# Kernel optimization log

Measured on AMD Instinct MI355X. Metric: run time of the kernel, lower is better.

## Reference

```python
import jax, jax.numpy as jnp
import numpy as np

B, CIN, H, W = 4, 256, 128, 128   # x1/x2 each [B, CIN, H, W]
C2 = 2 * CIN                       # 512, channels after concat
CQK = CIN // 8                     # 32, query/key channels


def setup_inputs() -> dict:
    key = jax.random.key(0)
    ks = jax.random.split(key, 12)
    s = 0.02
    return {
        "x1": jax.random.normal(ks[0], (B, CIN, H, W), jnp.float32),
        "x2": jax.random.normal(ks[1], (B, CIN, H, W), jnp.float32),
        # 1x1 convs as [out,in] matrices + bias
        "Wq": jax.random.normal(ks[2], (CQK, C2), jnp.float32) * s,
        "bq": jnp.zeros((CQK,), jnp.float32),
        "Wk": jax.random.normal(ks[3], (CQK, C2), jnp.float32) * s,
        "bk": jnp.zeros((CQK,), jnp.float32),
        "Wv": jax.random.normal(ks[4], (C2, C2), jnp.float32) * s,
        "bv": jnp.zeros((C2,), jnp.float32),
        "Wm": jax.random.normal(ks[5], (C2, C2), jnp.float32) * s,
        "bm": jnp.zeros((C2,), jnp.float32),
        "gamma": jnp.zeros((1,), jnp.float32),
    }


def _conv1x1(w, b, x):
    # x: [b,c,h,w] -> [b,o,h,w]
    return jnp.einsum('oc,bchw->bohw', w, x) + b[None, :, None, None]


def reference(x1, x2, Wq, bq, Wk, bk, Wv, bv, Wm, bm, gamma):
    b, _, h, w = x1.shape
    x = jnp.concatenate([x1, x2], axis=1)          # [b, 2C, h, w]
    q = _conv1x1(Wq, bq, x)                        # [b, cqk, h, w]
    k = _conv1x1(Wk, bk, x)                        # [b, cqk, h, w]
    v = _conv1x1(Wv, bv, x)                        # [b, 2C, h, w]

    # column (H-axis) energy: [b, h_q, w, h_k], diagonal h_q==h_k masked to -inf
    energy_H = jnp.einsum('bciw,bcjw->biwj', q, k)
    diag = jnp.eye(h, dtype=bool)[None, :, None, :]
    energy_H = jnp.where(diag, -jnp.inf, energy_H)
    # row (W-axis) energy: [b, h, w_q, w_k]
    energy_W = jnp.einsum('bchi,bchj->bhij', q, k)

    concate = jax.nn.softmax(jnp.concatenate([energy_H, energy_W], axis=3), axis=3)
    att_H = concate[..., :h]                       # [b, h_q, w, h_k]
    att_W = concate[..., h:]                       # [b, h, w_q, w_k]

    out_H = jnp.einsum('bcjw,biwj->bciw', v, att_H)  # [b, 2C, h, w]
    out_W = jnp.einsum('bchj,bhij->bchi', v, att_W)  # [b, 2C, h, w]

    out = gamma[0] * (out_H + out_W) + x
    out = _conv1x1(Wm, bm, out)                    # [b, 2C, h, w]
    out = out.reshape(b, 2, C2 // 2, h, w).transpose(1, 0, 2, 3, 4)
    return out
```

## Files before the change

### kernel.cpp

```cpp
#include <hip/hip_runtime.h>
#include <cstdint>

#define HW 16384
#define HH 128
#define WW 128
#define C2 512
#define CQK 32
#define NB_TOT 4

typedef unsigned short u16;
typedef unsigned int u32;

using bf16x8 = __attribute__((ext_vector_type(8))) short;
using f32x4  = __attribute__((ext_vector_type(4))) float;

__device__ __forceinline__ float us2f(u16 u) { return __uint_as_float(((u32)u) << 16); }
__device__ __forceinline__ u16 f2us(float f) {
    u32 u = __float_as_uint(f);
    u = u + 0x7fffu + ((u >> 16) & 1u);
    return (u16)(u >> 16);
}
__device__ __forceinline__ u32 pack2(float a, float b) {
    return (u32)f2us(a) | ((u32)f2us(b) << 16);
}
__device__ __forceinline__ void unpack8(uint4 p, float* f) {
    u32 a[4] = {p.x, p.y, p.z, p.w};
#pragma unroll
    for (int q = 0; q < 4; ++q) {
        f[q * 2 + 0] = __uint_as_float(a[q] << 16);
        f[q * 2 + 1] = __uint_as_float(a[q] & 0xffff0000u);
    }
}
union U8 { uint4 v; u16 s[8]; };

__device__ __forceinline__ void gl_lds16(const void* g, const void* lds) {
    __builtin_amdgcn_global_load_lds(
        (const __attribute__((address_space(1))) unsigned int*)g,
        (__attribute__((address_space(3))) unsigned int*)lds, 16, 0, 0);
}

__global__ __launch_bounds__(256) void convert_weights(
    const float* __restrict__ Wq, const float* __restrict__ Wk,
    const float* __restrict__ Wv, const float* __restrict__ Wm,
    u16* __restrict__ Wall)
{
    int id = blockIdx.x * 256 + threadIdx.x;
    if (id >= 1088 * 128) return;
    int row = id >> 7, q4 = id & 127;
    const float* src;
    if (row < 32) src = Wq + (size_t)row * 512;
    else if (row < 64) src = Wk + (size_t)(row - 32) * 512;
    else if (row < 576) src = Wv + (size_t)(row - 64) * 512;
    else src = Wm + (size_t)(row - 576) * 512;
    float4 v = *reinterpret_cast<const float4*>(src + q4 * 4);
    alignas(8) u16 h[4] = {f2us(v.x), f2us(v.y), f2us(v.z), f2us(v.w)};
    *reinterpret_cast<uint2*>(Wall + (size_t)row * 512 + q4 * 4) =
        *reinterpret_cast<uint2*>(h);
}

__global__ __launch_bounds__(512) void conv_final(
    const u16* __restrict__ Wmb, const float* __restrict__ bm,
    const float* __restrict__ x1, const float* __restrict__ x2,
    const u16* __restrict__ y, float* __restrict__ out,
    int b0, const float* __restrict__ gamma)
{
    __shared__ u16 As[512 * 64];
    __shared__ u32 Ps[64 * 36];
    const int t = threadIdx.x, lane = t & 63, wid = t >> 6;
    const int bz = blockIdx.z, bg = b0 + bz;
    const int p0 = blockIdx.x * 64;
    const int l15 = lane & 15, l16 = lane >> 4;
    const bool useY = (gamma[0] != 0.f);
    const int pcol = t & 15, cpair = t >> 4;
    const u16* yb = y + (size_t)bz * C2 * HW;

    f32x4 acc[4][4];
#pragma unroll
    for (int i = 0; i < 4; ++i)
#pragma unroll
        for (int j = 0; j < 4; ++j) acc[i][j] = (f32x4)0.f;

    for (int k0 = 0; k0 < 512; k0 += 64) {
        __syncthreads();
#pragma unroll
        for (int it = 0; it < 8; ++it) {
            int sflat = it * 512 + t;
            int m = sflat >> 3, slot = sflat & 7;
            int ck = slot ^ (m & 7);
            gl_lds16(Wmb + (size_t)m * 512 + k0 + ck * 8, As + sflat * 8);
        }
        {
            const int ce = k0 + cpair * 2, co = ce + 1;
            if (useY) {
                const u16* s0 = yb + (size_t)ce * HW + p0;
                const u16* s1 = yb + (size_t)co * HW + p0;
#pragma unroll
                for (int i = 0; i < 4; ++i) {
                    int p = pcol + i * 16;
                    Ps[p * 36 + cpair] = (u32)s0[p] | ((u32)s1[p] << 16);
                }
            } else {
                const float* s0 = (ce < 256) ? x1 + ((size_t)bg * 256 + ce) * HW + p0
                                             : x2 + ((size_t)bg * 256 + ce - 256) * HW + p0;
                const float* s1 = (co < 256) ? x1 + ((size_t)bg * 256 + co) * HW + p0
                                             : x2 + ((size_t)bg * 256 + co - 256) * HW + p0;
#pragma unroll
                for (int i = 0; i < 4; ++i) {
                    int p = pcol + i * 16;
                    Ps[p * 36 + cpair] = pack2(s0[p], s1[p]);
                }
            }
        }
        __syncthreads();
#pragma unroll
        for (int kk = 0; kk < 2; ++kk) {
            bf16x8 af[4], bfq[4];
#pragma unroll
            for (int mi = 0; mi < 4; ++mi) {
                int row = wid * 64 + mi * 16 + l15;
                int slot = (kk * 4 + l16) ^ (row & 7);
                af[mi] = *(const bf16x8*)&As[row * 64 + slot * 8];
            }
#pragma unroll
            for (int ni = 0; ni < 4; ++ni) {
                int p = ni * 16 + l15;
                bfq[ni] = *(const bf16x8*)((const u16*)&Ps[p * 36 + kk * 16 + l16 * 4]);
            }
#pragma unroll
            for (int mi = 0; mi < 4; ++mi)
#pragma unroll
                for (int ni = 0; ni < 4; ++ni)
                    acc[mi][ni] = __builtin_amdgcn_mfma_f32_16x16x32_bf16(
                        af[mi], bfq[ni], acc[mi][ni], 0, 0, 0);
        }
    }
#pragma unroll
    for (int mi = 0; mi < 4; ++mi)
#pragma unroll
        for (int ni = 0; ni < 4; ++ni) {
            const int p = p0 + ni * 16 + l15;
#pragma unroll
            for (int r = 0; r < 4; ++r) {
                const int m = wid * 64 + mi * 16 + l16 * 4 + r;
                const float val = acc[mi][ni][r] + bm[m];
                out[(((size_t)(m >> 8) * NB_TOT + bg) * 256 + (m & 255)) * HW + p] = val;
            }
        }
}

__global__ __launch_bounds__(256) void transpose_x(
    const float* __restrict__ x1, const float* __restrict__ x2,
    u16* __restrict__ xT, int b0, const float* __restrict__ gamma)
{
    if (gamma[0] == 0.f) return;
    __shared__ u16 tile[32][33];
    const int bz = blockIdx.z, bg = b0 + bz;
    const int p0 = blockIdx.x * 32;
    const int tx = threadIdx.x, ty = threadIdx.y;
    for (int cy = 0; cy < 16; ++cy) {
        const int c0 = cy * 32;
#pragma unroll
        for (int u = 0; u < 4; ++u) {
            int c = c0 + ty + u * 8;
            const float* xs = (c < 256) ? x1 + ((size_t)bg * 256 + c) * HW
                                        : x2 + ((size_t)bg * 256 + (c - 256)) * HW;
            tile[ty + u * 8][tx] = f2us(xs[p0 + tx]);
        }
        __syncthreads();
#pragma unroll
        for (int u = 0; u < 4; ++u) {
            int p = p0 + ty + u * 8;
            xT[((size_t)bz * HW + p) * 512 + c0 + tx] = tile[tx][ty + u * 8];
        }
        __syncthreads();
    }
}

template <int BM, int MODE>
__global__ __launch_bounds__(256) void conv_mfma(
    const u16* __restrict__ Wb, const float* __restrict__ bias0,
    const float* __restrict__ bias1, const u16* __restrict__ xT,
    float* __restrict__ oQ, float* __restrict__ oK,
    u16* __restrict__ oV, int b0, const float* __restrict__ gamma)
{
    if (gamma[0] == 0.f) return;
    constexpr int FM = BM / 32;
    __shared__ u16 As[BM * 64];
    __shared__ u16 Ps[128 * 64];
    const int t = threadIdx.x, lane = t & 63, wid = t >> 6;
    const int wr = wid >> 1, wc = wid & 1;
    const int bz = blockIdx.z;
    const int p0 = blockIdx.x * 128, m0 = blockIdx.y * BM;
    const u16* xTb = xT + (size_t)bz * HW * 512;
    const int l15 = lane & 15, l16 = lane >> 4;

    f32x4 acc[FM][4];
#pragma unroll
    for (int i = 0; i < FM; ++i)
#pragma unroll
        for (int j = 0; j < 4; ++j) acc[i][j] = (f32x4)0.f;

    for (int c0 = 0; c0 < 512; c0 += 64) {
#pragma unroll
        for (int it = 0; it < BM / 32; ++it) {
            int flat = it * 256 + t;
            int row = flat >> 3, part = flat & 7;
            gl_lds16(Wb + (size_t)(m0 + row) * 512 + c0 + part * 8,
                     As + (it * 256 + wid * 64) * 8);
        }
#pragma unroll
        for (int it = 0; it < 4; ++it) {
            int flat = it * 256 + t;
            int row = flat >> 3, part = flat & 7;
            gl_lds16(xTb + (size_t)(p0 + row) * 512 + c0 + part * 8,
                     Ps + (it * 256 + wid * 64) * 8);
        }
        __syncthreads();
#pragma unroll
        for (int kk = 0; kk < 2; ++kk) {
            bf16x8 af[FM], bfr[4];
#pragma unroll
            for (int mi = 0; mi < FM; ++mi)
                af[mi] = *(const bf16x8*)&As[(wr * (BM / 2) + mi * 16 + l15) * 64 + kk * 32 + l16 * 8];
#pragma unroll
            for (int ni = 0; ni < 4; ++ni)
                bfr[ni] = *(const bf16x8*)&Ps[(wc * 64 + ni * 16 + l15) * 64 + kk * 32 + l16 * 8];
#pragma unroll
            for (int mi = 0; mi < FM; ++mi)
#pragma unroll
                for (int ni = 0; ni < 4; ++ni)
                    acc[mi][ni] = __builtin_amdgcn_mfma_f32_16x16x32_bf16(
                        af[mi], bfr[ni], acc[mi][ni], 0, 0, 0);
        }
        __syncthreads();
    }
#pragma unroll
    for (int mi = 0; mi < FM; ++mi)
#pragma unroll
        for (int ni = 0; ni < 4; ++ni) {
            const int p = p0 + wc * 64 + ni * 16 + l15;
#pragma unroll
            for (int r = 0; r < 4; ++r) {
                const int m = m0 + wr * (BM / 2) + mi * 16 + l16 * 4 + r;
                float val = acc[mi][ni][r];
                if (MODE == 0) {
                    if (m < 32) {
                        val += bias0[m];
                        oQ[((size_t)bz * 32 + m) * HW + p] = val;
                    } else {
                        val += bias1[m - 32];
                        oK[((size_t)bz * 32 + (m - 32)) * HW + p] = val;
                    }
                } else {
                    val += bias0[m];
                    oV[((size_t)bz * 512 + m) * HW + p] = f2us(val);
                }
            }
        }
}

__global__ __launch_bounds__(256) void transpose_bf16(
    const u16* __restrict__ in, u16* __restrict__ out,
    const float* __restrict__ gamma)
{
    if (gamma[0] == 0.f) return;
    __shared__ u16 tile[32][33];
    const int x0 = blockIdx.x * 32, y0 = blockIdx.y * 32;
    const int tx = threadIdx.x, ty = threadIdx.y;
    for (int pp = 0; pp < 16; ++pp) {
        const int plane = blockIdx.z * 16 + pp;
        const u16* ip = in + (size_t)plane * HW;
        u16* op = out + (size_t)plane * HW;
#pragma unroll
        for (int u = 0; u < 4; ++u)
            tile[ty + u * 8][tx] = ip[(size_t)(y0 + ty + u * 8) * WW + x0 + tx];
        __syncthreads();
#pragma unroll
        for (int u = 0; u < 4; ++u)
            op[(size_t)(x0 + ty + u * 8) * HH + y0 + tx] = tile[tx][ty + u * 8];
        __syncthreads();
    }
}

__global__ __launch_bounds__(256) void energy_h_kernel(
    const float* __restrict__ q, const float* __restrict__ k,
    u16* __restrict__ EHt, const float* __restrict__ gamma)
{
    if (gamma[0] == 0.f) return;
    const int w = blockIdx.x, bz = blockIdx.y, t = threadIdx.x;
    __shared__ float qc[32][128];
    __shared__ float kc[32][128];
    __shared__ u16 es[128][128];
    for (int it = 0; it < 16; ++it) {
        int idx = it * 256 + t;
        int c = idx >> 7, j = idx & 127;
        qc[c][j] = q[((size_t)bz * CQK + c) * HW + j * WW + w];
        kc[c][j] = k[((size_t)bz * CQK + c) * HW + j * WW + w];
    }
    __syncthreads();
    const int i = t & 127, half = t >> 7, j0 = half * 64;
    float qi[32];
#pragma unroll
    for (int c = 0; c < 32; ++c) qi[c] = qc[c][i];
    for (int j = j0; j < j0 + 64; ++j) {
        float acc = 0.f;
#pragma unroll
        for (int c = 0; c < 32; ++c) acc += qi[c] * kc[c][j];
        es[i][j] = f2us(i == j ? -1e30f : acc);
    }
    __syncthreads();
    u16* dst = EHt + ((size_t)bz * WW + w) * HW;
    for (int it = 0; it < 8; ++it) {
        int ii = it * 16 + (t >> 4), jj = (t & 15) * 8;
        *reinterpret_cast<uint4*>(&dst[(size_t)ii * HH + jj]) =
            *reinterpret_cast<const uint4*>(&es[ii][jj]);
    }
}

__global__ __launch_bounds__(256) void ew_softmax_ow_kernel(
    const float* __restrict__ q, const float* __restrict__ k,
    const u16* __restrict__ v, u16* __restrict__ EHt,
    u16* __restrict__ oW, const float* __restrict__ gamma)
{
    if (gamma[0] == 0.f) return;
    const int r = blockIdx.x, bz = blockIdx.y, t = threadIdx.x;
    __shared__ float qr[32][128];
    __shared__ float kr[32][128];
    __shared__ u16 ewT[128][136];
    __shared__ u16 vstageT[128][40];
    __shared__ float invA[128];
    __shared__ float red[2][2][128];

    for (int it = 0; it < 16; ++it) {
        int idx = it * 256 + t, c = idx >> 7, j = idx & 127;
        qr[c][j] = q[((size_t)bz * CQK + c) * HW + r * WW + j];
        kr[c][j] = k[((size_t)bz * CQK + c) * HW + r * WW + j];
    }
    __syncthreads();
    const int i = t & 127, half = t >> 7, j0 = half * 64;
    {
        float qi[32];
#pragma unroll
        for (int c = 0; c < 32; ++c) qi[c] = qr[c][i];
        for (int j = j0; j < j0 + 64; ++j) {
            float acc = 0.f;
#pragma unroll
            for (int c = 0; c < 32; ++c) acc += qi[c] * kr[c][j];
            ewT[j][i] = f2us(acc);
        }
    }
    __syncthreads();
    float eh[64];
    u16* ehrow = EHt + (((size_t)bz * WW + i) * HH + r) * HH + j0;
#pragma unroll
    for (int uq = 0; uq < 8; ++uq) {
        uint4 pk = *reinterpret_cast<const uint4*>(ehrow + uq * 8);
        unpack8(pk, eh + uq * 8);
    }
    float m = -3e38f;
#pragma unroll
    for (int u = 0; u < 64; ++u) m = fmaxf(m, eh[u]);
    for (int j = j0; j < j0 + 64; ++j) m = fmaxf(m, us2f(ewT[j][i]));
    red[0][half][i] = m;
    __syncthreads();
    m = fmaxf(red[0][0][i], red[0][1][i]);
    float s = 0.f;
#pragma unroll
    for (int u = 0; u < 64; ++u) { float e = __expf(eh[u] - m); eh[u] = e; s += e; }
    for (int j = j0; j < j0 + 64; ++j) {
        float e = __expf(us2f(ewT[j][i]) - m);
        ewT[j][i] = f2us(e);
        s += e;
    }
    red[1][half][i] = s;
    __syncthreads();
    const float inv = 1.f / (red[1][0][i] + red[1][1][i]);
    if (half == 0) invA[i] = inv;
#pragma unroll
    for (int uq = 0; uq < 8; ++uq) {
        alignas(16) u16 tmp[8];
#pragma unroll
        for (int e = 0; e < 8; ++e) tmp[e] = f2us(eh[uq * 8 + e] * inv);
        *reinterpret_cast<uint4*>(ehrow + uq * 8) = *reinterpret_cast<uint4*>(tmp);
    }
    const int cg = half;
    for (int c0 = 0; c0 < C2; c0 += 32) {
        __syncthreads();
        for (int it = 0; it < 16; ++it) {
            int idx = it * 256 + t, cc = idx >> 7, j = idx & 127;
            vstageT[j][cc] = v[((size_t)bz * C2 + c0 + cc) * HW + r * WW + j];
        }
        __syncthreads();
        float acc[16] = {};
        for (int j = 0; j < 128; ++j) {
            float a = us2f(ewT[j][i]);
            uint4 pq0 = *reinterpret_cast<const uint4*>(&vstageT[j][cg * 16]);
            uint4 pq1 = *reinterpret_cast<const uint4*>(&vstageT[j][cg * 16 + 8]);
            float vv[16];
            unpack8(pq0, vv);
            unpack8(pq1, vv + 8);
#pragma unroll
            for (int u = 0; u < 16; ++u) acc[u] += a * vv[u];
        }
        const float scale = invA[i];
#pragma unroll
        for (int u = 0; u < 16; ++u) {
            int c = c0 + cg * 16 + u;
            oW[((size_t)bz * C2 + c) * HW + r * WW + i] = f2us(acc[u] * scale);
        }
    }
}

__global__ __launch_bounds__(256) void apply_h_kernel(
    const u16* __restrict__ EHt, const u16* __restrict__ vT,
    u16* __restrict__ oHT, const float* __restrict__ gamma)
{
    if (gamma[0] == 0.f) return;
    const int w = blockIdx.x, bz = blockIdx.y, t = threadIdx.x;
    __shared__ u16 aT[128][136];
    __shared__ u16 vstageT[128][40];
    const u16* src = EHt + ((size_t)bz * WW + w) * HW;
    for (int it = 0; it < 8; ++it) {
        int oct = it * 256 + t;
        int ii = oct >> 4, jj = (oct & 15) * 8;
        U8 uu;
        uu.v = *reinterpret_cast<const uint4*>(src + (size_t)ii * HH + jj);
#pragma unroll
        for (int e = 0; e < 8; ++e) aT[jj + e][ii] = uu.s[e];
    }
    const int i = t & 127, cg = t >> 7;
    for (int c0 = 0; c0 < C2; c0 += 32) {
        __syncthreads();
        for (int it = 0; it < 16; ++it) {
            int idx = it * 256 + t, cc = idx >> 7, j = idx & 127;
            vstageT[j][cc] = vT[((size_t)bz * C2 + c0 + cc) * HW + w * HH + j];
        }
        __syncthreads();
        float acc[16] = {};
        for (int j = 0; j < 128; ++j) {
            float a = us2f(aT[j][i]);
            uint4 pq0 = *reinterpret_cast<const uint4*>(&vstageT[j][cg * 16]);
            uint4 pq1 = *reinterpret_cast<const uint4*>(&vstageT[j][cg * 16 + 8]);
            float vv[16];
            unpack8(pq0, vv);
            unpack8(pq1, vv + 8);
#pragma unroll
            for (int u = 0; u < 16; ++u) acc[u] += a * vv[u];
        }
#pragma unroll
        for (int u = 0; u < 16; ++u) {
            int c = c0 + cg * 16 + u;
            oHT[((size_t)bz * C2 + c) * HW + w * HH + i] = f2us(acc[u]);
        }
    }
}

__global__ __launch_bounds__(256) void merge_transpose_kernel(
    const u16* __restrict__ oHT, const u16* __restrict__ oW,
    const float* __restrict__ x1, const float* __restrict__ x2,
    const float* __restrict__ gamma, u16* __restrict__ y, int b0)
{
    const float g = gamma[0];
    if (g == 0.f) return;
    __shared__ float tile[32][33];
    const int w0 = blockIdx.x * 32, i0 = blockIdx.y * 32;
    const int tx = threadIdx.x, ty = threadIdx.y;
    for (int pp = 0; pp < 16; ++pp) {
        const int idx = blockIdx.z * 16 + pp;
        const int c = idx & 511, bz = idx >> 9;
        const int bg = b0 + bz;
        const u16* ih = oHT + ((size_t)bz * C2 + c) * HW;
#pragma unroll
        for (int u = 0; u < 4; ++u)
            tile[ty + u * 8][tx] = us2f(ih[(size_t)(w0 + ty + u * 8) * HH + i0 + tx]);
        __syncthreads();
        const float* xs = (c < 256) ? (x1 + ((size_t)bg * 256 + c) * HW)
                                    : (x2 + ((size_t)bg * 256 + (c - 256)) * HW);
        const u16* ow = oW + ((size_t)bz * C2 + c) * HW;
        u16* yy = y + ((size_t)bz * C2 + c) * HW;
#pragma unroll
        for (int u = 0; u < 4; ++u) {
            int i = i0 + ty + u * 8, w = w0 + tx;
            float oh = tile[tx][ty + u * 8];
            float val = g * (oh + us2f(ow[(size_t)i * WW + w])) + xs[(size_t)i * WW + w];
            yy[(size_t)i * WW + w] = f2us(val);
        }
        __syncthreads();
    }
}

extern "C" void kernel_launch(void* const* d_in, const int* in_sizes, int n_in,
                              void* d_out, int out_size, void* d_ws, size_t ws_size,
                              hipStream_t stream)
{
    const float* x1 = (const float*)d_in[0];
    const float* x2 = (const float*)d_in[1];
    const float* Wq = (const float*)d_in[2];
    const float* bq = (const float*)d_in[3];
    const float* Wk = (const float*)d_in[4];
    const float* bk = (const float*)d_in[5];
    const float* Wv = (const float*)d_in[6];
    const float* bv = (const float*)d_in[7];
    const float* Wm = (const float*)d_in[8];
    const float* bm = (const float*)d_in[9];
    const float* gamma = (const float*)d_in[10];
    float* out = (float*)d_out;

    auto algn = [](size_t v) { return (v + 255) & ~(size_t)255; };
    const size_t wallSz = algn((size_t)1088 * 512 * 2);
    auto need = [&](int nb) -> size_t {
        size_t s = wallSz;
        s += algn((size_t)nb * HW * 512 * 2);
        s += 2 * algn((size_t)nb * 32 * HW * 4);
        s += algn((size_t)nb * C2 * HW * 2);
        s += algn((size_t)nb * C2 * HW * 2);
        s += algn((size_t)nb * WW * HW * 2);
        s += algn((size_t)nb * C2 * HW * 2);
        s += algn((size_t)nb * C2 * HW * 2);
        return s;
    };
    const int nb = (ws_size >= need(4)) ? 4 : (ws_size >= need(2)) ? 2 : 1;

    char* base = (char*)d_ws;
    u16* Wall = (u16*)base; base += wallSz;
    const u16* Wqk = Wall;
    const u16* Wvb = Wall + (size_t)64 * 512;
    const u16* Wmb = Wall + (size_t)576 * 512;

    convert_weights<<<(1088 * 128 + 255) / 256, 256, 0, stream>>>(Wq, Wk, Wv, Wm, Wall);

    for (int b0 = 0; b0 < NB_TOT; b0 += nb) {
        char* p = base;
        u16* xT   = (u16*)p;   p += algn((size_t)nb * HW * 512 * 2);
        float* q  = (float*)p; p += algn((size_t)nb * 32 * HW * 4);
        float* kk = (float*)p; p += algn((size_t)nb * 32 * HW * 4);
        u16* v    = (u16*)p;   p += algn((size_t)nb * C2 * HW * 2);
        u16* vT   = (u16*)p;   p += algn((size_t)nb * C2 * HW * 2);
        u16* EHt  = (u16*)p;   p += algn((size_t)nb * WW * HW * 2);
        u16* oW   = (u16*)p;   p += algn((size_t)nb * C2 * HW * 2);
        u16* oHT  = (u16*)p;   p += algn((size_t)nb * C2 * HW * 2);
        u16* y    = vT;

        transpose_x<<<dim3(HW / 32, 1, nb), dim3(32, 8), 0, stream>>>(
            x1, x2, xT, b0, gamma);
        conv_mfma<64, 0><<<dim3(HW / 128, 1, nb), 256, 0, stream>>>(
            Wqk, bq, bk, xT, q, kk, nullptr, b0, gamma);
        conv_mfma<128, 1><<<dim3(HW / 128, 4, nb), 256, 0, stream>>>(
            Wvb, bv, nullptr, xT, nullptr, nullptr, v, b0, gamma);
        transpose_bf16<<<dim3(4, 4, nb * 32), dim3(32, 8), 0, stream>>>(v, vT, gamma);
        energy_h_kernel<<<dim3(WW, nb), 256, 0, stream>>>(q, kk, EHt, gamma);
        ew_softmax_ow_kernel<<<dim3(HH, nb), 256, 0, stream>>>(q, kk, v, EHt, oW, gamma);
        apply_h_kernel<<<dim3(WW, nb), 256, 0, stream>>>(EHt, vT, oHT, gamma);
        merge_transpose_kernel<<<dim3(4, 4, nb * 32), dim3(32, 8), 0, stream>>>(
            oHT, oW, x1, x2, gamma, y, b0);
        conv_final<<<dim3(HW / 64, 1, nb), 512, 0, stream>>>(
            Wmb, bm, x1, x2, y, out, b0, gamma);
    }
}
```

Measured before the change: 104.0 us.

## Double-buffer weight tiles and widen pixel tile in final conv

The final 1x1 conv kernel now processes 128 pixels per block instead of 64, doubling the accumulator tile per wave so each loaded weight fragment is reused across twice as many MFMAs. It also double-buffers the weight tile in LDS and prefetches the next activation slice into registers while the current slice is being multiplied, hiding global load latency behind compute. The cost is much larger LDS use (two 64KB weight buffers), more accumulator and staging registers, and half as many blocks, all of which may reduce occupancy.

```diff
diff --git a/kernel.cpp b/kernel.cpp
--- a/kernel.cpp
+++ b/kernel.cpp
@@ -64,86 +64,110 @@
     const u16* __restrict__ y, float* __restrict__ out,
     int b0, const float* __restrict__ gamma)
 {
-    __shared__ u16 As[512 * 64];
-    __shared__ u32 Ps[64 * 36];
+    __shared__ u16 As[2][512 * 64];
+    __shared__ u32 Ps[128 * 36];
     const int t = threadIdx.x, lane = t & 63, wid = t >> 6;
     const int bz = blockIdx.z, bg = b0 + bz;
-    const int p0 = blockIdx.x * 64;
+    const int p0 = blockIdx.x * 128;
     const int l15 = lane & 15, l16 = lane >> 4;
     const bool useY = (gamma[0] != 0.f);
     const int pcol = t & 15, cpair = t >> 4;
     const u16* yb = y + (size_t)bz * C2 * HW;
 
-    f32x4 acc[4][4];
+    f32x4 acc[4][8];
 #pragma unroll
     for (int i = 0; i < 4; ++i)
 #pragma unroll
-        for (int j = 0; j < 4; ++j) acc[i][j] = (f32x4)0.f;
-
-    for (int k0 = 0; k0 < 512; k0 += 64) {
-        __syncthreads();
+        for (int j = 0; j < 8; ++j) acc[i][j] = (f32x4)0.f;
+
+    u32 xr[16];
+
+    auto stageW = [&](int k0, int b) {
 #pragma unroll
         for (int it = 0; it < 8; ++it) {
             int sflat = it * 512 + t;
             int m = sflat >> 3, slot = sflat & 7;
             int ck = slot ^ (m & 7);
-            gl_lds16(Wmb + (size_t)m * 512 + k0 + ck * 8, As + sflat * 8);
-        }
-        {
-            const int ce = k0 + cpair * 2, co = ce + 1;
-            if (useY) {
-                const u16* s0 = yb + (size_t)ce * HW + p0;
-                const u16* s1 = yb + (size_t)co * HW + p0;
-#pragma unroll
-                for (int i = 0; i < 4; ++i) {
-                    int p = pcol + i * 16;
-                    Ps[p * 36 + cpair] = (u32)s0[p] | ((u32)s1[p] << 16);
-                }
-            } else {
-                const float* s0 = (ce < 256) ? x1 + ((size_t)bg * 256 + ce) * HW + p0
-                                             : x2 + ((size_t)bg * 256 + ce - 256) * HW + p0;
-                const float* s1 = (co < 256) ? x1 + ((size_t)bg * 256 + co) * HW + p0
-                                             : x2 + ((size_t)bg * 256 + co - 256) * HW + p0;
-#pragma unroll
-                for (int i = 0; i < 4; ++i) {
-                    int p = pcol + i * 16;
-                    Ps[p * 36 + cpair] = pack2(s0[p], s1[p]);
-                }
+            gl_lds16(Wmb + (size_t)m * 512 + k0 + ck * 8, &As[b][sflat * 8]);
+        }
+    };
+    auto loadX = [&](int k0) {
+        const int ce = k0 + cpair * 2;
+        if (useY) {
+            const u16* s0 = yb + (size_t)ce * HW + p0;
+            const u16* s1 = s0 + HW;
+#pragma unroll
+            for (int i = 0; i < 8; ++i) {
+                int p = pcol + i * 16;
+                xr[i] = s0[p]; xr[8 + i] = s1[p];
             }
-        }
-        __syncthreads();
+        } else {
+            const float* s0 = (ce < 256) ? x1 + ((size_t)bg * 256 + ce) * HW + p0
+                                         : x2 + ((size_t)bg * 256 + ce - 256) * HW + p0;
+            const float* s1 = s0 + HW;
+#pragma unroll
+            for (int i = 0; i < 8; ++i) {
+                int p = pcol + i * 16;
+                xr[i] = __float_as_uint(s0[p]);
+                xr[8 + i] = __float_as_uint(s1[p]);
+            }
+        }
+    };
+    auto writeX = [&]() {
+#pragma unroll
+        for (int i = 0; i < 8; ++i) {
+            int p = pcol + i * 16;
+            u32 d = useY ? (xr[i] | (xr[8 + i] << 16))
+                         : pack2(__uint_as_float(xr[i]), __uint_as_float(xr[8 + i]));
+            Ps[p * 36 + cpair] = d;
+        }
+    };
+
+    stageW(0, 0);
+    loadX(0);
+    writeX();
+    __syncthreads();
+
+    for (int k = 0; k < 8; ++k) {
+        const int cb = k & 1;
+        if (k < 7) {
+            stageW((k + 1) * 64, cb ^ 1);
+            loadX((k + 1) * 64);
+        }
 #pragma unroll
         for (int kk = 0; kk < 2; ++kk) {
-            bf16x8 af[4], bfq[4];
+            bf16x8 af[4];
 #pragma unroll
             for (int mi = 0; mi < 4; ++mi) {
                 int row = wid * 64 + mi * 16 + l15;
                 int slot = (kk * 4 + l16) ^ (row & 7);
-                af[mi] = *(const bf16x8*)&As[row * 64 + slot * 8];
+                af[mi] = *(const bf16x8*)&As[cb][row * 64 + slot * 8];
             }
 #pragma unroll
-            for (int ni = 0; ni < 4; ++ni) {
-                int p = ni * 16 + l15;
-                bfq[ni] = *(const bf16x8*)((const u16*)&Ps[p * 36 + kk * 16 + l16 * 4]);
+            for (int ni = 0; ni < 8; ++ni) {
+                bf16x8 bq = *(const bf16x8*)((const u16*)&Ps[(ni * 16 + l15) * 36 + kk * 16 + l16 * 4]);
+#pragma unroll
+                for (int mi = 0; mi < 4; ++mi)
+                    acc[mi][ni] = __builtin_amdgcn_mfma_f32_16x16x32_bf16(
+                        af[mi], bq, acc[mi][ni], 0, 0, 0);
             }
-#pragma unroll
-            for (int mi = 0; mi < 4; ++mi)
-#pragma unroll
-                for (int ni = 0; ni < 4; ++ni)
-                    acc[mi][ni] = __builtin_amdgcn_mfma_f32_16x16x32_bf16(
-                        af[mi], bfq[ni], acc[mi][ni], 0, 0, 0);
+        }
+        __syncthreads();
+        if (k < 7) {
+            writeX();
+            __syncthreads();
         }
     }
 #pragma unroll
     for (int mi = 0; mi < 4; ++mi)
 #pragma unroll
-        for (int ni = 0; ni < 4; ++ni) {
+        for (int ni = 0; ni < 8; ++ni) {
             const int p = p0 + ni * 16 + l15;
 #pragma unroll
             for (int r = 0; r < 4; ++r) {
                 const int m = wid * 64 + mi * 16 + l16 * 4 + r;
-                const float val = acc[mi][ni][r] + bm[m];
-                out[(((size_t)(m >> 8) * NB_TOT + bg) * 256 + (m & 255)) * HW + p] = val;
+                out[(((size_t)(m >> 8) * NB_TOT + bg) * 256 + (m & 255)) * HW + p] =
+                    acc[mi][ni][r] + bm[m];
             }
         }
 }
@@ -553,7 +577,7 @@
         apply_h_kernel<<<dim3(WW, nb), 256, 0, stream>>>(EHt, vT, oHT, gamma);
         merge_transpose_kernel<<<dim3(4, 4, nb * 32), dim3(32, 8), 0, stream>>>(
             oHT, oW, x1, x2, gamma, y, b0);
-        conv_final<<<dim3(HW / 64, 1, nb), 512, 0, stream>>>(
+        conv_final<<<dim3(HW / 128, 1, nb), 512, 0, stream>>>(
             Wmb, bm, x1, x2, y, out, b0, gamma);
     }
 }
```

Measured after the change: 87.62 us. 15.8% less time.

## Split conv_final output channels across blocks and batch global loads into registers

Applied to the files above, without the earlier changes.

The final 1x1 conv kernel now uses 256-thread blocks that each cover 256 output channels, with a second grid dimension over channel halves. Each wave computes a 128x32 tile instead of 64x64. The weight LDS tile is halved, and launch bounds request 3 blocks per CU for more occupancy. Activation loads for a k-step are gathered into registers before being packed and written to LDS, which lets the loads overlap. In exchange, every activation tile is now loaded twice, once per channel half.

```diff
diff --git a/kernel.cpp b/kernel.cpp
--- a/kernel.cpp
+++ b/kernel.cpp
@@ -58,92 +58,108 @@
         *reinterpret_cast<uint2*>(h);
 }
 
-__global__ __launch_bounds__(512) void conv_final(
+__global__ __launch_bounds__(256, 3) void conv_final(
     const u16* __restrict__ Wmb, const float* __restrict__ bm,
     const float* __restrict__ x1, const float* __restrict__ x2,
     const u16* __restrict__ y, float* __restrict__ out,
     int b0, const float* __restrict__ gamma)
 {
-    __shared__ u16 As[512 * 64];
+    __shared__ u16 As[256 * 64];
     __shared__ u32 Ps[64 * 36];
     const int t = threadIdx.x, lane = t & 63, wid = t >> 6;
+    const int wr = wid >> 1, wc = wid & 1;
     const int bz = blockIdx.z, bg = b0 + bz;
-    const int p0 = blockIdx.x * 64;
+    const int p0 = blockIdx.x * 64, m0 = blockIdx.y * 256;
     const int l15 = lane & 15, l16 = lane >> 4;
     const bool useY = (gamma[0] != 0.f);
     const int pcol = t & 15, cpair = t >> 4;
     const u16* yb = y + (size_t)bz * C2 * HW;
 
-    f32x4 acc[4][4];
-#pragma unroll
-    for (int i = 0; i < 4; ++i)
-#pragma unroll
-        for (int j = 0; j < 4; ++j) acc[i][j] = (f32x4)0.f;
+    f32x4 acc[8][2];
+#pragma unroll
+    for (int i = 0; i < 8; ++i)
+#pragma unroll
+        for (int j = 0; j < 2; ++j) acc[i][j] = (f32x4)0.f;
 
     for (int k0 = 0; k0 < 512; k0 += 64) {
-        __syncthreads();
 #pragma unroll
         for (int it = 0; it < 8; ++it) {
-            int sflat = it * 512 + t;
+            int sflat = it * 256 + t;
             int m = sflat >> 3, slot = sflat & 7;
             int ck = slot ^ (m & 7);
-            gl_lds16(Wmb + (size_t)m * 512 + k0 + ck * 8, As + sflat * 8);
-        }
-        {
-            const int ce = k0 + cpair * 2, co = ce + 1;
+            gl_lds16(Wmb + (size_t)(m0 + m) * 512 + k0 + ck * 8, As + sflat * 8);
+        }
+        u32 xr[16];
+#pragma unroll
+        for (int g = 0; g < 2; ++g) {
+            const int cp = cpair + g * 16;
+            const int ce = k0 + cp * 2;
             if (useY) {
                 const u16* s0 = yb + (size_t)ce * HW + p0;
-                const u16* s1 = yb + (size_t)co * HW + p0;
+                const u16* s1 = s0 + HW;
 #pragma unroll
                 for (int i = 0; i < 4; ++i) {
                     int p = pcol + i * 16;
-                    Ps[p * 36 + cpair] = (u32)s0[p] | ((u32)s1[p] << 16);
+                    xr[g * 8 + i * 2] = s0[p];
+                    xr[g * 8 + i * 2 + 1] = s1[p];
                 }
             } else {
                 const float* s0 = (ce < 256) ? x1 + ((size_t)bg * 256 + ce) * HW + p0
                                              : x2 + ((size_t)bg * 256 + ce - 256) * HW + p0;
-                const float* s1 = (co < 256) ? x1 + ((size_t)bg * 256 + co) * HW + p0
-                                             : x2 + ((size_t)bg * 256 + co - 256) * HW + p0;
+                const float* s1 = ((ce + 1) < 256) ? x1 + ((size_t)bg * 256 + ce + 1) * HW + p0
+                                                   : x2 + ((size_t)bg * 256 + ce + 1 - 256) * HW + p0;
 #pragma unroll
                 for (int i = 0; i < 4; ++i) {
                     int p = pcol + i * 16;
-                    Ps[p * 36 + cpair] = pack2(s0[p], s1[p]);
+                    xr[g * 8 + i * 2] = __float_as_uint(s0[p]);
+                    xr[g * 8 + i * 2 + 1] = __float_as_uint(s1[p]);
                 }
             }
         }
+#pragma unroll
+        for (int g = 0; g < 2; ++g)
+#pragma unroll
+            for (int i = 0; i < 4; ++i) {
+                int p = pcol + i * 16;
+                u32 d = useY ? (xr[g * 8 + i * 2] | (xr[g * 8 + i * 2 + 1] << 16))
+                             : pack2(__uint_as_float(xr[g * 8 + i * 2]),
+                                     __uint_as_float(xr[g * 8 + i * 2 + 1]));
+                Ps[p * 36 + cpair + g * 16] = d;
+            }
         __syncthreads();
 #pragma unroll
         for (int kk = 0; kk < 2; ++kk) {
-            bf16x8 af[4], bfq[4];
-#pragma unroll
-            for (int mi = 0; mi < 4; ++mi) {
-                int row = wid * 64 + mi * 16 + l15;
+            bf16x8 af[8], bq[2];
+#pragma unroll
+            for (int mi = 0; mi < 8; ++mi) {
+                int row = wr * 128 + mi * 16 + l15;
                 int slot = (kk * 4 + l16) ^ (row & 7);
                 af[mi] = *(const bf16x8*)&As[row * 64 + slot * 8];
             }
 #pragma unroll
-            for (int ni = 0; ni < 4; ++ni) {
-                int p = ni * 16 + l15;
-                bfq[ni] = *(const bf16x8*)((const u16*)&Ps[p * 36 + kk * 16 + l16 * 4]);
+            for (int ni = 0; ni < 2; ++ni) {
+                int p = wc * 32 + ni * 16 + l15;
+                bq[ni] = *(const bf16x8*)((const u16*)&Ps[p * 36 + kk * 16 + l16 * 4]);
             }
 #pragma unroll
-            for (int mi = 0; mi < 4; ++mi)
-#pragma unroll
-                for (int ni = 0; ni < 4; ++ni)
+            for (int mi = 0; mi < 8; ++mi)
+#pragma unroll
+                for (int ni = 0; ni < 2; ++ni)
                     acc[mi][ni] = __builtin_amdgcn_mfma_f32_16x16x32_bf16(
-                        af[mi], bfq[ni], acc[mi][ni], 0, 0, 0);
-        }
-    }
-#pragma unroll
-    for (int mi = 0; mi < 4; ++mi)
-#pragma unroll
-        for (int ni = 0; ni < 4; ++ni) {
-            const int p = p0 + ni * 16 + l15;
+                        af[mi], bq[ni], acc[mi][ni], 0, 0, 0);
+        }
+        __syncthreads();
+    }
+#pragma unroll
+    for (int mi = 0; mi < 8; ++mi)
+#pragma unroll
+        for (int ni = 0; ni < 2; ++ni) {
+            const int p = p0 + wc * 32 + ni * 16 + l15;
 #pragma unroll
             for (int r = 0; r < 4; ++r) {
-                const int m = wid * 64 + mi * 16 + l16 * 4 + r;
-                const float val = acc[mi][ni][r] + bm[m];
-                out[(((size_t)(m >> 8) * NB_TOT + bg) * 256 + (m & 255)) * HW + p] = val;
+                const int m = m0 + wr * 128 + mi * 16 + l16 * 4 + r;
+                out[(((size_t)(m >> 8) * NB_TOT + bg) * 256 + (m & 255)) * HW + p] =
+                    acc[mi][ni][r] + bm[m];
             }
         }
 }
@@ -553,7 +569,7 @@
         apply_h_kernel<<<dim3(WW, nb), 256, 0, stream>>>(EHt, vT, oHT, gamma);
         merge_transpose_kernel<<<dim3(4, 4, nb * 32), dim3(32, 8), 0, stream>>>(
             oHT, oW, x1, x2, gamma, y, b0);
-        conv_final<<<dim3(HW / 64, 1, nb), 512, 0, stream>>>(
+        conv_final<<<dim3(HW / 64, 2, nb), 256, 0, stream>>>(
             Wmb, bm, x1, x2, y, out, b0, gamma);
     }
 }
```

Result: faster. 90.93 us (-12.6%).
